# Kernel optimization log

Measured on AMD Instinct MI355X. Metric: run time of the kernel, lower is better.

## Reference

```python
import jax, jax.numpy as jnp
import numpy as np
from jax import lax

V, E, H, L, T, B = 50000, 512, 1024, 2, 512, 64


def _lstm_layer(x_seq, h0, c0, W_ih, W_hh):
    # x_seq: [T, B, D_in]; W_ih: [4H, D_in]; W_hh: [4H, H]
    x_proj = jnp.einsum('tbd,gd->tbg', x_seq, W_ih)  # precompute input projection

    def step(carry, xp):
        h, c = carry
        gates = xp + h @ W_hh.T  # [B, 4H], PyTorch gate order i,f,g,o
        i, f, g, o = jnp.split(gates, 4, axis=-1)
        i = jax.nn.sigmoid(i)
        f = jax.nn.sigmoid(f)
        g = jnp.tanh(g)
        o = jax.nn.sigmoid(o)
        c = f * c + i * g
        h = o * jnp.tanh(c)
        return (h, c), h

    (hT, cT), ys = lax.scan(step, (h0, c0), x_proj)
    return ys, hT, cT


def setup_inputs() -> dict:
    key = jax.random.key(0)
    ks = jax.random.split(key, 8)
    inputs = jax.random.randint(ks[0], (T, B), 0, V)
    h0 = jnp.zeros((L, B, H), jnp.float32)
    c0 = jnp.zeros((L, B, H), jnp.float32)
    emb = jax.random.uniform(ks[1], (V, E), jnp.float32, -0.1, 0.1)
    s_ih0 = 1.0 / np.sqrt(H)
    W_ih0 = jax.random.uniform(ks[2], (4 * H, E), jnp.float32, -s_ih0, s_ih0)
    W_hh0 = jax.random.uniform(ks[3], (4 * H, H), jnp.float32, -s_ih0, s_ih0)
    W_ih1 = jax.random.uniform(ks[4], (4 * H, H), jnp.float32, -s_ih0, s_ih0)
    W_hh1 = jax.random.uniform(ks[5], (4 * H, H), jnp.float32, -s_ih0, s_ih0)
    dec_W = jax.random.uniform(ks[6], (1, H), jnp.float32, -0.1, 0.1)
    dec_b = jnp.zeros((1,), jnp.float32)
    return {"inputs": inputs, "h0": h0, "c0": c0, "emb": emb,
            "W_ih0": W_ih0, "W_hh0": W_hh0, "W_ih1": W_ih1, "W_hh1": W_hh1,
            "dec_W": dec_W, "dec_b": dec_b}


def reference(inputs, h0, c0, emb, W_ih0, W_hh0, W_ih1, W_hh1, dec_W, dec_b):
    x = emb[inputs]                                      # [T, B, E]
    y0, h1, c1 = _lstm_layer(x, h0[0], c0[0], W_ih0, W_hh0)   # [T, B, H]
    # dropout between layers is inference-disabled (eval mode)
    y1, h2, c2 = _lstm_layer(y0, h0[1], c0[1], W_ih1, W_hh1)  # [T, B, H]
    pooled = jnp.mean(y1, axis=0)                        # [B, H] (squeeze is a no-op)
    decoded = pooled @ dec_W.T + dec_b                   # [B, 1]
    hn = jnp.stack([h1, h2])
    cn = jnp.stack([c1, c2])
    return decoded, hn, cn
```

## Files before the change

### kernel.cpp

```cpp
#include <hip/hip_runtime.h>

#define TT 512
#define BB 64
#define HH 1024
#define EE 512
#define VV 50000
#define BBHH (BB*HH)
#define BPL 128
#define NBLK 256

typedef __attribute__((ext_vector_type(8))) short bf16x8;
typedef __attribute__((ext_vector_type(4))) float f32x4;
typedef unsigned short us;

#define MFMA(a,b,c) __builtin_amdgcn_mfma_f32_16x16x32_bf16((a),(b),(c),0,0,0)
#define LDG(p) __hip_atomic_load((p), __ATOMIC_RELAXED, __HIP_MEMORY_SCOPE_AGENT)

__device__ inline us f2b(float f){
  unsigned u; __builtin_memcpy(&u, &f, 4);
  return (us)((u + 0x7FFFu + ((u >> 16) & 1u)) >> 16);
}
__device__ inline float sigmoidf_(float x){ return 1.0f / (1.0f + __expf(-x)); }
__device__ inline float tanhf_(float x){ float e = __expf(2.0f * x); return 1.0f - 2.0f / (e + 1.0f); }

__device__ inline bf16x8 pack8(float4 a, float4 b){
  bf16x8 r;
  r[0]=(short)f2b(a.x); r[1]=(short)f2b(a.y); r[2]=(short)f2b(a.z); r[3]=(short)f2b(a.w);
  r[4]=(short)f2b(b.x); r[5]=(short)f2b(b.y); r[6]=(short)f2b(b.z); r[7]=(short)f2b(b.w);
  return r;
}

__global__ void cast_f2b(const float* __restrict__ src, us* __restrict__ dst, long n){
  long i = ((long)blockIdx.x * blockDim.x + threadIdx.x) * 4;
  long stride = (long)gridDim.x * blockDim.x * 4;
  for (; i + 3 < n; i += stride){
    float4 v = *reinterpret_cast<const float4*>(src + i);
    ushort4 r; r.x=f2b(v.x); r.y=f2b(v.y); r.z=f2b(v.z); r.w=f2b(v.w);
    *reinterpret_cast<ushort4*>(dst + i) = r;
  }
}

__global__ void init_h(const float* __restrict__ h0,
                       us* __restrict__ h0ic, us* __restrict__ h1ic){
  int i = blockIdx.x * blockDim.x + threadIdx.x;
  int b = i >> 10, j = i & (HH - 1);
  int d = (((j >> 3) * BB) + b) * 8 + (j & 7);
  h0ic[d] = f2b(h0[i]);
  h1ic[d] = f2b(h0[BBHH + i]);
}

__device__ __forceinline__ void wait_win(const unsigned* __restrict__ f, int base,
                                         unsigned e, int lane){
  const unsigned* p = f + base + (lane & 31);
  unsigned a = LDG(p);
  while (!__all((int)(a >= e))){
    __builtin_amdgcn_s_sleep(8);
    a = LDG(p);
  }
}

__device__ __forceinline__ void publish(unsigned* __restrict__ f, int bid_l, unsigned e){
  asm volatile("s_waitcnt vmcnt(0)" ::: "memory");
  __syncthreads();
  if (threadIdx.x == 0)
    __hip_atomic_store(f + bid_l, e, __ATOMIC_RELAXED, __HIP_MEMORY_SCOPE_AGENT);
}

#define LIDX(m, s) ((((m) * 16 + (s)) * 64 + lane) * 4)

#define CBASE ((wid * 32 + hi) * (BB * 8) + l16 * 8)

__device__ void run_l0(
    int bid_l, int lane, int wid, int l16, int hi, int kq,
    const int* __restrict__ inputs, const float* __restrict__ c0,
    const us* __restrict__ emb_bf,
    const float* __restrict__ Wih0, const float* __restrict__ Whh0,
    const us* __restrict__ h0ic,
    us* __restrict__ hist0,
    float* __restrict__ hn, float* __restrict__ cn,
    unsigned* __restrict__ flags0, float* lds)
{
  const int j0 = bid_l * 8;
  const int bown = wid * 16 + l16;
  const int cbase = CBASE;
  const int wbase = wid * 32;

  bf16x8 wx[2][4], wh[2][8];
  #pragma unroll
  for (int m = 0; m < 2; ++m){
    const int g = l16 & 3;
    const int u = 2 * (l16 >> 2) + m;
    const float* rx = Wih0 + (size_t)(g * HH + j0 + u) * EE;
    const float* rh = Whh0 + (size_t)(g * HH + j0 + u) * HH;
    #pragma unroll
    for (int kk = 0; kk < 4; ++kk){
      int k0 = wid * 128 + kk * 32 + kq;
      wx[m][kk] = pack8(*reinterpret_cast<const float4*>(rx + k0),
                        *reinterpret_cast<const float4*>(rx + k0 + 4));
    }
    #pragma unroll
    for (int kk = 0; kk < 8; ++kk){
      int k0 = wid * 256 + kk * 32 + kq;
      wh[m][kk] = pack8(*reinterpret_cast<const float4*>(rh + k0),
                        *reinterpret_cast<const float4*>(rh + k0 + 4));
    }
  }

  float cs[2];
  #pragma unroll
  for (int m = 0; m < 2; ++m)
    cs[m] = c0[(size_t)bown * HH + j0 + 2 * hi + m];

  for (int t = 0; t < TT; ++t){
    f32x4 acc[2][4];
    #pragma unroll
    for (int m = 0; m < 2; ++m)
      #pragma unroll
      for (int nt = 0; nt < 4; ++nt)
        acc[m][nt] = (f32x4){0.f,0.f,0.f,0.f};

    {
      const us* xr[4];
      #pragma unroll
      for (int nt = 0; nt < 4; ++nt)
        xr[nt] = emb_bf + (size_t)inputs[t * BB + nt * 16 + l16] * EE;
      #pragma unroll
      for (int kk = 0; kk < 4; ++kk){
        const int kb = wid * 128 + kk * 32 + kq;
        #pragma unroll
        for (int nt = 0; nt < 4; ++nt){
          bf16x8 bf = *reinterpret_cast<const bf16x8*>(xr[nt] + kb);
          acc[0][nt] = MFMA(wx[0][kk], bf, acc[0][nt]);
          acc[1][nt] = MFMA(wx[1][kk], bf, acc[1][nt]);
        }
      }
    }

    if (t > 0) wait_win(flags0, wbase, (unsigned)t, lane);

    {
      const us* hs = (t == 0) ? h0ic : hist0 + (size_t)(t - 1) * BBHH;
      #pragma unroll
      for (int kk = 0; kk < 8; ++kk){
        #pragma unroll
        for (int nt = 0; nt < 4; ++nt){
          bf16x8 bf = *reinterpret_cast<const bf16x8*>(hs + cbase + kk * 2048 + nt * 128);
          acc[0][nt] = MFMA(wh[0][kk], bf, acc[0][nt]);
          acc[1][nt] = MFMA(wh[1][kk], bf, acc[1][nt]);
        }
      }
    }

    #pragma unroll
    for (int m = 0; m < 2; ++m)
      #pragma unroll
      for (int nt = 0; nt < 4; ++nt)
        *reinterpret_cast<f32x4*>(&lds[LIDX(m, wid * 4 + nt)]) = acc[m][nt];
    __syncthreads();
    f32x4 s[2];
    #pragma unroll
    for (int m = 0; m < 2; ++m){
      s[m] = (f32x4){0.f,0.f,0.f,0.f};
      #pragma unroll
      for (int w = 0; w < 4; ++w)
        s[m] += *reinterpret_cast<f32x4*>(&lds[LIDX(m, w * 4 + wid)]);
    }

    float hv[2];
    #pragma unroll
    for (int m = 0; m < 2; ++m){
      float gi = sigmoidf_(s[m][0]), gf = sigmoidf_(s[m][1]);
      float gg = tanhf_(s[m][2]),    go = sigmoidf_(s[m][3]);
      cs[m] = gf * cs[m] + gi * gg;
      hv[m] = go * tanhf_(cs[m]);
    }
    unsigned w = (unsigned)f2b(hv[0]) | ((unsigned)f2b(hv[1]) << 16);
    __hip_atomic_store(reinterpret_cast<unsigned*>(hist0 + (size_t)t * BBHH + (size_t)(bid_l * BB + bown) * 8 + 2 * hi),
                       w, __ATOMIC_RELAXED, __HIP_MEMORY_SCOPE_AGENT);
    if (t == TT - 1){
      size_t o = (size_t)bown * HH + j0 + 2 * hi;
      *reinterpret_cast<float2*>(hn + o) = make_float2(hv[0], hv[1]);
      *reinterpret_cast<float2*>(cn + o) = make_float2(cs[0], cs[1]);
    }

    publish(flags0, bid_l, (unsigned)(t + 1));
  }
}

__device__ void run_l1(
    int bid_l, int lane, int wid, int l16, int hi, int kq,
    const float* __restrict__ c0,
    const float* __restrict__ Wih1, const float* __restrict__ Whh1,
    const us* __restrict__ h1ic,
    const us* __restrict__ hist0, us* __restrict__ hist1,
    const float* __restrict__ decW, const float* __restrict__ decb,
    float* __restrict__ dec_out, float* __restrict__ hn, float* __restrict__ cn,
    unsigned* __restrict__ flags0, unsigned* __restrict__ flags1, float* lds)
{
  const int j0 = bid_l * 8;
  const int bown = wid * 16 + l16;
  const int cbase = CBASE;
  const int wbase = wid * 32;

  bf16x8 wx[2][8], wh[2][8];
  #pragma unroll
  for (int m = 0; m < 2; ++m){
    const int g = l16 & 3;
    const int u = 2 * (l16 >> 2) + m;
    const float* rx = Wih1 + (size_t)(g * HH + j0 + u) * HH;
    const float* rh = Whh1 + (size_t)(g * HH + j0 + u) * HH;
    #pragma unroll
    for (int kk = 0; kk < 8; ++kk){
      int k0 = wid * 256 + kk * 32 + kq;
      wx[m][kk] = pack8(*reinterpret_cast<const float4*>(rx + k0),
                        *reinterpret_cast<const float4*>(rx + k0 + 4));
      wh[m][kk] = pack8(*reinterpret_cast<const float4*>(rh + k0),
                        *reinterpret_cast<const float4*>(rh + k0 + 4));
    }
  }

  float cs[2];
  #pragma unroll
  for (int m = 0; m < 2; ++m)
    cs[m] = c0[(size_t)BBHH + (size_t)bown * HH + j0 + 2 * hi + m];
  float pooldec = 0.0f;
  const float dwv0 = decW[j0 + 2 * hi], dwv1 = decW[j0 + 2 * hi + 1];

  for (int t = 0; t < TT; ++t){
    f32x4 acc[2][4];
    #pragma unroll
    for (int m = 0; m < 2; ++m)
      #pragma unroll
      for (int nt = 0; nt < 4; ++nt)
        acc[m][nt] = (f32x4){0.f,0.f,0.f,0.f};

    if (t > 0) wait_win(flags1, wbase, (unsigned)t, lane);
    {
      const us* hs = (t == 0) ? h1ic : hist1 + (size_t)(t - 1) * BBHH;
      #pragma unroll
      for (int kk = 0; kk < 8; ++kk){
        #pragma unroll
        for (int nt = 0; nt < 4; ++nt){
          bf16x8 bf = *reinterpret_cast<const bf16x8*>(hs + cbase + kk * 2048 + nt * 128);
          acc[0][nt] = MFMA(wh[0][kk], bf, acc[0][nt]);
          acc[1][nt] = MFMA(wh[1][kk], bf, acc[1][nt]);
        }
      }
    }

    wait_win(flags0, wbase, (unsigned)(t + 1), lane);
    {
      const us* xs = hist0 + (size_t)t * BBHH;
      #pragma unroll
      for (int kk = 0; kk < 8; ++kk){
        #pragma unroll
        for (int nt = 0; nt < 4; ++nt){
          bf16x8 bf = *reinterpret_cast<const bf16x8*>(xs + cbase + kk * 2048 + nt * 128);
          acc[0][nt] = MFMA(wx[0][kk], bf, acc[0][nt]);
          acc[1][nt] = MFMA(wx[1][kk], bf, acc[1][nt]);
        }
      }
    }

    #pragma unroll
    for (int m = 0; m < 2; ++m)
      #pragma unroll
      for (int nt = 0; nt < 4; ++nt)
        *reinterpret_cast<f32x4*>(&lds[LIDX(m, wid * 4 + nt)]) = acc[m][nt];
    __syncthreads();
    f32x4 s[2];
    #pragma unroll
    for (int m = 0; m < 2; ++m){
      s[m] = (f32x4){0.f,0.f,0.f,0.f};
      #pragma unroll
      for (int w = 0; w < 4; ++w)
        s[m] += *reinterpret_cast<f32x4*>(&lds[LIDX(m, w * 4 + wid)]);
    }

    float hv[2];
    #pragma unroll
    for (int m = 0; m < 2; ++m){
      float gi = sigmoidf_(s[m][0]), gf = sigmoidf_(s[m][1]);
      float gg = tanhf_(s[m][2]),    go = sigmoidf_(s[m][3]);
      cs[m] = gf * cs[m] + gi * gg;
      hv[m] = go * tanhf_(cs[m]);
    }
    unsigned w = (unsigned)f2b(hv[0]) | ((unsigned)f2b(hv[1]) << 16);
    __hip_atomic_store(reinterpret_cast<unsigned*>(hist1 + (size_t)t * BBHH + (size_t)(bid_l * BB + bown) * 8 + 2 * hi),
                       w, __ATOMIC_RELAXED, __HIP_MEMORY_SCOPE_AGENT);
    pooldec += hv[0] * dwv0 + hv[1] * dwv1;
    if (t == TT - 1){
      size_t o = (size_t)BBHH + (size_t)bown * HH + j0 + 2 * hi;
      *reinterpret_cast<float2*>(hn + o) = make_float2(hv[0], hv[1]);
      *reinterpret_cast<float2*>(cn + o) = make_float2(cs[0], cs[1]);
    }

    publish(flags1, bid_l, (unsigned)(t + 1));
  }

  pooldec += __shfl_xor(pooldec, 16);
  pooldec += __shfl_xor(pooldec, 32);
  if (hi == 0){
    float contrib = pooldec * (1.0f / (float)TT);
    if (bid_l == 0) contrib += decb[0];
    atomicAdd(&dec_out[bown], contrib);
  }
}

__global__ __launch_bounds__(256, 1) void lstm_persist(
    const int* __restrict__ inputs, const float* __restrict__ c0,
    const us* __restrict__ emb_bf,
    const float* __restrict__ Wih0, const float* __restrict__ Whh0,
    const float* __restrict__ Wih1, const float* __restrict__ Whh1,
    const us* __restrict__ h0ic, const us* __restrict__ h1ic,
    us* __restrict__ hist0, us* __restrict__ hist1,
    const float* __restrict__ decW, const float* __restrict__ decb,
    float* __restrict__ dec_out, float* __restrict__ hn, float* __restrict__ cn,
    unsigned* __restrict__ flags)
{
  __shared__ float lds[2 * 16 * 64 * 4];
  const int tid  = threadIdx.x;
  const int lane = tid & 63;
  const int wid  = tid >> 6;
  const int l16  = lane & 15;
  const int hi   = lane >> 4;
  const int kq   = hi << 3;
  unsigned* flags0 = flags;
  unsigned* flags1 = flags + 128;

  int bid = blockIdx.x;
  if (bid < BPL){
    run_l0(bid, lane, wid, l16, hi, kq, inputs, c0, emb_bf, Wih0, Whh0,
           h0ic, hist0, hn, cn, flags0, lds);
  } else {
    run_l1(bid - BPL, lane, wid, l16, hi, kq, c0, Wih1, Whh1,
           h1ic, hist0, hist1, decW, decb, dec_out, hn, cn, flags0, flags1, lds);
  }
}

extern "C" void kernel_launch(void* const* d_in, const int* in_sizes, int n_in,
                              void* d_out, int out_size, void* d_ws, size_t ws_size,
                              hipStream_t stream){
  const int*   inputs = (const int*)d_in[0];
  const float* h0     = (const float*)d_in[1];
  const float* c0     = (const float*)d_in[2];
  const float* emb    = (const float*)d_in[3];
  const float* Wih0   = (const float*)d_in[4];
  const float* Whh0   = (const float*)d_in[5];
  const float* Wih1   = (const float*)d_in[6];
  const float* Whh1   = (const float*)d_in[7];
  const float* decW   = (const float*)d_in[8];
  const float* decb   = (const float*)d_in[9];

  char* ws = (char*)d_ws;
  size_t off = 0;
  auto alloc = [&](size_t bytes) -> void* {
    void* p = ws + off;
    off += (bytes + 255) & ~(size_t)255;
    return p;
  };
  us* emb_bf = (us*)alloc((size_t)VV * EE * 2);
  us* hist0  = (us*)alloc((size_t)TT * BBHH * 2);
  us* hist1  = (us*)alloc((size_t)TT * BBHH * 2);
  us* h0ic   = (us*)alloc((size_t)BBHH * 2);
  us* h1ic   = (us*)alloc((size_t)BBHH * 2);
  unsigned* flags = (unsigned*)alloc((size_t)256 * 4);

  float* out = (float*)d_out;
  float* hn  = out + BB;
  float* cn  = out + BB + 2 * BBHH;

  hipMemsetAsync(flags, 0, 256 * 4, stream);
  hipMemsetAsync(out, 0, BB * 4, stream);

  cast_f2b<<<2048, 256, 0, stream>>>(emb, emb_bf, (long)VV * EE);
  init_h<<<BBHH / 256, 256, 0, stream>>>(h0, h0ic, h1ic);

  lstm_persist<<<NBLK, 256, 0, stream>>>(inputs, c0, emb_bf,
                                         Wih0, Whh0, Wih1, Whh1,
                                         h0ic, h1ic, hist0, hist1,
                                         decW, decb, out, hn, cn, flags);
}
```

Before: 4.154 ms.

## Replace per-block barrier publish with per-wave flags and double-buffer LDS reduction

Each wave now publishes its own completion flag after its global stores drain, instead of every block paying an extra __syncthreads before one thread writes a block flag. Waiters poll 128 per-wave flags (two loads per lane) rather than 32 block flags. The LDS gate-reduction scratch is double-buffered by timestep parity, so dropping the trailing barrier cannot let one step's writes race the previous step's reads. The cost is four times more flags, wider polling traffic, and twice the LDS.

```diff
diff --git a/kernel.cpp b/kernel.cpp
--- a/kernel.cpp
+++ b/kernel.cpp
@@ -49,24 +49,25 @@
   h1ic[d] = f2b(h0[BBHH + i]);
 }
 
-__device__ __forceinline__ void wait_win(const unsigned* __restrict__ f, int base,
+__device__ __forceinline__ void wait_win(const unsigned* __restrict__ f, int wbase,
                                          unsigned e, int lane){
-  const unsigned* p = f + base + (lane & 31);
-  unsigned a = LDG(p);
-  while (!__all((int)(a >= e))){
+  const unsigned* p = f + wbase;
+  unsigned a = LDG(p + lane), b = LDG(p + 64 + lane);
+  while (!__all((int)(a >= e && b >= e))){
     __builtin_amdgcn_s_sleep(8);
-    a = LDG(p);
-  }
-}
-
-__device__ __forceinline__ void publish(unsigned* __restrict__ f, int bid_l, unsigned e){
+    a = LDG(p + lane); b = LDG(p + 64 + lane);
+  }
+}
+
+__device__ __forceinline__ void wave_flag(unsigned* __restrict__ f, int idx,
+                                          unsigned e, int lane){
   asm volatile("s_waitcnt vmcnt(0)" ::: "memory");
-  __syncthreads();
-  if (threadIdx.x == 0)
-    __hip_atomic_store(f + bid_l, e, __ATOMIC_RELAXED, __HIP_MEMORY_SCOPE_AGENT);
+  if (lane == 0)
+    __hip_atomic_store(f + idx, e, __ATOMIC_RELAXED, __HIP_MEMORY_SCOPE_AGENT);
 }
 
 #define LIDX(m, s) ((((m) * 16 + (s)) * 64 + lane) * 4)
+#define ZHALF 8192
 
 #define CBASE ((wid * 32 + hi) * (BB * 8) + l16 * 8)
 
@@ -78,12 +79,13 @@
     const us* __restrict__ h0ic,
     us* __restrict__ hist0,
     float* __restrict__ hn, float* __restrict__ cn,
-    unsigned* __restrict__ flags0, float* lds)
+    unsigned* __restrict__ flags0, float* zone)
 {
   const int j0 = bid_l * 8;
   const int bown = wid * 16 + l16;
   const int cbase = CBASE;
-  const int wbase = wid * 32;
+  const int wbase = wid * 128;
+  const int fidx  = bid_l * 4 + wid;
 
   bf16x8 wx[2][4], wh[2][8];
   #pragma unroll
@@ -112,6 +114,7 @@
     cs[m] = c0[(size_t)bown * HH + j0 + 2 * hi + m];
 
   for (int t = 0; t < TT; ++t){
+    float* zb = zone + (t & 1) * ZHALF;
     f32x4 acc[2][4];
     #pragma unroll
     for (int m = 0; m < 2; ++m)
@@ -155,7 +158,7 @@
     for (int m = 0; m < 2; ++m)
       #pragma unroll
       for (int nt = 0; nt < 4; ++nt)
-        *reinterpret_cast<f32x4*>(&lds[LIDX(m, wid * 4 + nt)]) = acc[m][nt];
+        *reinterpret_cast<f32x4*>(&zb[LIDX(m, wid * 4 + nt)]) = acc[m][nt];
     __syncthreads();
     f32x4 s[2];
     #pragma unroll
@@ -163,7 +166,7 @@
       s[m] = (f32x4){0.f,0.f,0.f,0.f};
       #pragma unroll
       for (int w = 0; w < 4; ++w)
-        s[m] += *reinterpret_cast<f32x4*>(&lds[LIDX(m, w * 4 + wid)]);
+        s[m] += *reinterpret_cast<f32x4*>(&zb[LIDX(m, w * 4 + wid)]);
     }
 
     float hv[2];
@@ -183,7 +186,7 @@
       *reinterpret_cast<float2*>(cn + o) = make_float2(cs[0], cs[1]);
     }
 
-    publish(flags0, bid_l, (unsigned)(t + 1));
+    wave_flag(flags0, fidx, (unsigned)(t + 1), lane);
   }
 }
 
@@ -195,12 +198,13 @@
     const us* __restrict__ hist0, us* __restrict__ hist1,
     const float* __restrict__ decW, const float* __restrict__ decb,
     float* __restrict__ dec_out, float* __restrict__ hn, float* __restrict__ cn,
-    unsigned* __restrict__ flags0, unsigned* __restrict__ flags1, float* lds)
+    unsigned* __restrict__ flags0, unsigned* __restrict__ flags1, float* zone)
 {
   const int j0 = bid_l * 8;
   const int bown = wid * 16 + l16;
   const int cbase = CBASE;
-  const int wbase = wid * 32;
+  const int wbase = wid * 128;
+  const int fidx  = bid_l * 4 + wid;
 
   bf16x8 wx[2][8], wh[2][8];
   #pragma unroll
@@ -227,6 +231,7 @@
   const float dwv0 = decW[j0 + 2 * hi], dwv1 = decW[j0 + 2 * hi + 1];
 
   for (int t = 0; t < TT; ++t){
+    float* zb = zone + (t & 1) * ZHALF;
     f32x4 acc[2][4];
     #pragma unroll
     for (int m = 0; m < 2; ++m)
@@ -266,7 +271,7 @@
     for (int m = 0; m < 2; ++m)
       #pragma unroll
       for (int nt = 0; nt < 4; ++nt)
-        *reinterpret_cast<f32x4*>(&lds[LIDX(m, wid * 4 + nt)]) = acc[m][nt];
+        *reinterpret_cast<f32x4*>(&zb[LIDX(m, wid * 4 + nt)]) = acc[m][nt];
     __syncthreads();
     f32x4 s[2];
     #pragma unroll
@@ -274,7 +279,7 @@
       s[m] = (f32x4){0.f,0.f,0.f,0.f};
       #pragma unroll
       for (int w = 0; w < 4; ++w)
-        s[m] += *reinterpret_cast<f32x4*>(&lds[LIDX(m, w * 4 + wid)]);
+        s[m] += *reinterpret_cast<f32x4*>(&zb[LIDX(m, w * 4 + wid)]);
     }
 
     float hv[2];
@@ -295,7 +300,7 @@
       *reinterpret_cast<float2*>(cn + o) = make_float2(cs[0], cs[1]);
     }
 
-    publish(flags1, bid_l, (unsigned)(t + 1));
+    wave_flag(flags1, fidx, (unsigned)(t + 1), lane);
   }
 
   pooldec += __shfl_xor(pooldec, 16);
@@ -318,7 +323,7 @@
     float* __restrict__ dec_out, float* __restrict__ hn, float* __restrict__ cn,
     unsigned* __restrict__ flags)
 {
-  __shared__ float lds[2 * 16 * 64 * 4];
+  __shared__ float zone[2 * ZHALF];
   const int tid  = threadIdx.x;
   const int lane = tid & 63;
   const int wid  = tid >> 6;
@@ -326,15 +331,15 @@
   const int hi   = lane >> 4;
   const int kq   = hi << 3;
   unsigned* flags0 = flags;
-  unsigned* flags1 = flags + 128;
+  unsigned* flags1 = flags + 512;
 
   int bid = blockIdx.x;
   if (bid < BPL){
     run_l0(bid, lane, wid, l16, hi, kq, inputs, c0, emb_bf, Wih0, Whh0,
-           h0ic, hist0, hn, cn, flags0, lds);
+           h0ic, hist0, hn, cn, flags0, zone);
   } else {
     run_l1(bid - BPL, lane, wid, l16, hi, kq, c0, Wih1, Whh1,
-           h1ic, hist0, hist1, decW, decb, dec_out, hn, cn, flags0, flags1, lds);
+           h1ic, hist0, hist1, decW, decb, dec_out, hn, cn, flags0, flags1, zone);
   }
 }
 
@@ -364,13 +369,13 @@
   us* hist1  = (us*)alloc((size_t)TT * BBHH * 2);
   us* h0ic   = (us*)alloc((size_t)BBHH * 2);
   us* h1ic   = (us*)alloc((size_t)BBHH * 2);
-  unsigned* flags = (unsigned*)alloc((size_t)256 * 4);
+  unsigned* flags = (unsigned*)alloc((size_t)1024 * 4);
 
   float* out = (float*)d_out;
   float* hn  = out + BB;
   float* cn  = out + BB + 2 * BBHH;
 
-  hipMemsetAsync(flags, 0, 256 * 4, stream);
+  hipMemsetAsync(flags, 0, 1024 * 4, stream);
   hipMemsetAsync(out, 0, BB * 4, stream);
 
   cast_f2b<<<2048, 256, 0, stream>>>(emb, emb_bf, (long)VV * EE);
```

New measurement: 4.646 ms. +11.8%, slower.
